# Performance work log

Measured on AMD Instinct MI355X. Metric: run time of the kernel, lower is better.

## Reference

```python
import jax, jax.numpy as jnp
import numpy as np

NB = 5          # LC kernel size (odd -> L_out == L with pad = NB//2)
S = 8           # num_sparse_LC segments
N_LEVELS = 4
K_DENSE = 3
K_LC = 3
SQ = np.float32(np.sqrt(0.5))


def haar_dec(x):
    # level-1 haar wavedec, periodization mode; x: (..., L), L even
    x0, x1 = x[..., 0::2], x[..., 1::2]
    return (x0 + x1) * SQ, (x0 - x1) * SQ  # (cA, cD)


def haar_rec(cA, cD):
    # inverse of haar_dec
    x0 = (cA + cD) * SQ
    x1 = (cA - cD) * SQ
    return jnp.stack([x0, x1], axis=-1).reshape(cA.shape[:-1] + (-1,))


def lc_apply(x, w, b):
    # cheapPartiallyUnsharedConv1d. x: (B,d,k,2,L); w: (d,k,o=2,i=2,S,NB); b: (d,k,2,S)
    L = x.shape[-1]
    p = NB // 2
    xp = jnp.pad(x, ((0, 0),) * 4 + ((p, p),))
    idx = jnp.arange(L)[:, None] + jnp.arange(NB)[None, :]      # (L, NB)
    patches = xp[..., idx]                                      # (B,d,k,2,L,NB)
    # per-segment weights: floor(L/S) repeats per segment, remainder -> last segment
    R = L // S
    seg = jnp.clip(jnp.arange(L) // R, 0, S - 1)                # (L,)
    wf = w[:, :, :, :, seg, :]                                  # (d,k,o,i,L,NB)
    bf = b[:, :, :, seg]                                        # (d,k,o,L)
    return jnp.einsum('dkoilf,bdkilf->bdkol', wf, patches) + bf


def lin_deriv(ts, ys, t):
    # derivative of linear interpolation of ys over knots ts, evaluated at t
    # ts: (T,); ys: (B,T,D); t: (T,) -> (B,T,D)
    i = jnp.clip(jnp.searchsorted(ts, t, side='right') - 1, 0, ts.shape[0] - 2)
    return (ys[:, i + 1, :] - ys[:, i, :]) / (ts[i + 1] - ts[i])[None, :, None]


def setup_inputs() -> dict:
    key = jax.random.key(0)
    ks = jax.random.split(key, 8)
    B, L, D, d, k = 16, 2048, 64, 32, 16
    dn = L >> N_LEVELS  # 128 == dense_dim
    seq = jax.random.normal(ks[0], (B, L, D), jnp.float32)
    coeffs = jax.random.normal(ks[1], (B, L, D), jnp.float32)
    time_step = jnp.arange(L, dtype=jnp.float32)
    time = jnp.arange(L, dtype=jnp.float32)
    Wg = jax.random.normal(ks[2], (D, d), jnp.float32) * (2.0 / D) ** 0.5
    Wh = jax.random.normal(ks[3], (d, D * k), jnp.float32) * (2.0 / d) ** 0.5
    dense_W = jax.random.normal(ks[4], (K_DENSE, d, k, dn, dn), jnp.float32) * (2.0 / dn) ** 0.5
    lc_w = jax.random.normal(ks[5], (N_LEVELS, K_LC, d, k, 2, 2, S, NB), jnp.float32) * (2.0 / (2 * NB)) ** 0.5
    lc_b = jax.random.uniform(ks[6], (N_LEVELS, K_LC, d, k, 2, S), jnp.float32)
    Wrev = jax.random.normal(ks[7], (d, D), jnp.float32) * (2.0 / d) ** 0.5
    return dict(seq=seq, coeffs=coeffs, time=time, time_step=time_step,
                Wg=Wg, Wh=Wh, dense_W=dense_W, lc_w=lc_w, lc_b=lc_b, Wrev=Wrev)


def reference(seq, coeffs, time, time_step, Wg, Wh, dense_W, lc_w, lc_b, Wrev):
    B, L, D = seq.shape
    d = Wg.shape[1]
    k = Wh.shape[1] // D
    der = lin_deriv(time_step, coeffs, time)                    # (B,L,D) == der_X.squeeze(-1)
    z = jax.nn.relu(seq @ Wg)                                   # (B,L,d)
    h = jax.nn.relu(z @ Wh).reshape(B, L, D, k)                 # (B,L,D,k)
    v = jnp.einsum('blDk,blD->bkl', h, der)                     # (B,k,L)

    # analysis: n_levels of level-1 haar wavedec
    ca = v
    details, approxs = [], []
    for _ in range(N_LEVELS):
        ca, cd = haar_dec(ca)
        details.append(cd)
        approxs.append(ca)

    # coarsest approx -> per-(d,k) dense stack
    cur = jnp.tile(approxs[-1][:, None, :, :], (1, d, 1, 1))    # (B,d,k,dn)
    for j in range(K_DENSE):
        cur = jnp.einsum('dktq,bdkq->bdkt', dense_W[j], cur)

    # synthesis with locally-connected refinements
    for l in reversed(range(N_LEVELS)):
        chi = jnp.tile(jnp.stack([details[l], approxs[l]], axis=2)[:, None],
                       (1, d, 1, 1, 1))                          # (B,d,k,2,Ll)
        for j in range(K_LC):
            chi = jax.nn.relu(lc_apply(chi, lc_w[l, j], lc_b[l, j]))
        # shape_correction is identity: lengths match exactly with haar/pow2
        X = chi.at[:, :, :, 1, :].add(cur)                       # add approx on channel 1
        cur = haar_rec(X[:, :, :, 1, :], X[:, :, :, 0, :])       # (B,d,k,2*Ll)

    out = jnp.sum(cur, axis=2)                                   # (B,d,L)
    U = jnp.transpose(out, (0, 2, 1)) @ Wrev                     # (B,L,D_out)
    return U
```

## Files before the change

kernel.cpp:

```cpp
#include <hip/hip_runtime.h>

#define SQC 0.70710678118654752f

typedef __attribute__((ext_vector_type(8))) short bf16x8;
typedef __attribute__((ext_vector_type(4))) float f32x4;

__device__ __forceinline__ unsigned short bf16_rne(float x) {
  unsigned int u = __float_as_uint(x);
  u += 0x7FFFu + ((u >> 16) & 1u);
  return (unsigned short)(u >> 16);
}

__global__ __launch_bounds__(256) void k_prep_all(const float* __restrict__ Wh,
                                                  unsigned short* __restrict__ WhT,
                                                  const float* __restrict__ lcw,
                                                  const float* __restrict__ lcb,
                                                  float* __restrict__ re) {
  int bid = blockIdx.x;
  if (bid < 128) {
    int i = bid * 256 + threadIdx.x;
    int n = i >> 5, dd = i & 31;
    WhT[i] = bf16_rne(Wh[dd * 1024 + n]);
    return;
  }
  int g = (bid - 128) * 256 + threadIdx.x;
  int l = g / 294912;
  int r1 = g - l * 294912;
  int dk = r1 / 576;
  int i = r1 - dk * 576;
  int j = i / 192;
  int r = i - j * 192;
  int sg = r / 24;
  int t = r - sg * 24;
  float val = 0.f;
  if (t < 20) {
    int oi = t / 5, f = t - oi * 5;
    val = lcw[((size_t)(l * 3 + j) * 512 + dk) * 160 + (oi * 8 + sg) * 5 + f];
  } else if (t < 22) {
    val = lcb[((size_t)(l * 3 + j) * 512 + dk) * 16 + (t - 20) * 8 + sg];
  }
  re[g] = val;
}

__global__ __launch_bounds__(256) void k_zv(const float* __restrict__ seq,
                                            const float* __restrict__ Wg,
                                            const float* __restrict__ coeffs,
                                            const unsigned short* __restrict__ WhT,
                                            float* __restrict__ v) {
  __shared__ unsigned short zs[64][40];
  __shared__ float ders[64][68];
  __shared__ float vout[16][68];
  const int tid = threadIdx.x;
  const int b = blockIdx.x >> 5;
  const int lblk = (blockIdx.x & 31) * 64;
  {
    const int r = tid >> 2;
    const int dq = tid & 3;
    const float4* srow = (const float4*)(seq + ((size_t)b * 2048 + lblk + r) * 64);
    float acc[8];
#pragma unroll
    for (int i = 0; i < 8; ++i) acc[i] = 0.f;
#pragma unroll 4
    for (int D4 = 0; D4 < 16; ++D4) {
      float4 s4 = srow[D4];
      const float* sp = (const float*)&s4;
#pragma unroll
      for (int q = 0; q < 4; ++q) {
        float s = sp[q];
        int D = D4 * 4 + q;
        const float* wr = Wg + D * 32 + dq * 8;
#pragma unroll
        for (int dd2 = 0; dd2 < 8; ++dd2) acc[dd2] = fmaf(s, wr[dd2], acc[dd2]);
      }
    }
    uint4 o;
    unsigned int* op = (unsigned int*)&o;
#pragma unroll
    for (int i = 0; i < 4; ++i) {
      unsigned int lo = bf16_rne(fmaxf(acc[2 * i], 0.f));
      unsigned int hi = bf16_rne(fmaxf(acc[2 * i + 1], 0.f));
      op[i] = lo | (hi << 16);
    }
    *(uint4*)&zs[r][dq * 8] = o;
  }
  for (int i = tid; i < 4096; i += 256) {
    int r = i >> 6, D = i & 63;
    int ii = min(lblk + r, 2046);
    const float* c0 = coeffs + ((size_t)b * 2048 + ii) * 64 + D;
    ders[r][D] = c0[64] - c0[0];
  }
  __syncthreads();
  const int lane = tid & 63;
  const int wv = tid >> 6;
  const int col = lane & 15, quad = lane >> 4;
  bf16x8 afrag = *(bf16x8*)&zs[wv * 16 + col][quad * 8];
  f32x4 vacc = {0.f, 0.f, 0.f, 0.f};
  const unsigned short* bptr = WhT + col * 32 + quad * 8;
  const int lrow0 = wv * 16 + quad * 4;
#pragma unroll 4
  for (int t = 0; t < 64; ++t) {
    bf16x8 bfrag = *(const bf16x8*)(bptr + t * 512);
    f32x4 c = {0.f, 0.f, 0.f, 0.f};
    c = __builtin_amdgcn_mfma_f32_16x16x32_bf16(afrag, bfrag, c, 0, 0, 0);
#pragma unroll
    for (int r = 0; r < 4; ++r)
      vacc[r] = fmaf(fmaxf(c[r], 0.f), ders[lrow0 + r][t], vacc[r]);
  }
#pragma unroll
  for (int r = 0; r < 4; ++r) vout[col][lrow0 + r] = vacc[r];
  __syncthreads();
  for (int i = tid; i < 1024; i += 256) {
    int kk = i >> 6, ll = i & 63;
    v[((size_t)b * 16 + kk) * 2048 + lblk + ll] = vout[kk][ll];
  }
}

__global__ __launch_bounds__(64) void k_haar(const float* __restrict__ v,
                                             float* __restrict__ wdet,
                                             float* __restrict__ wapp,
                                             float* __restrict__ a0T) {
  const int bk = blockIdx.x;
  const int L = threadIdx.x;
  const float* src = v + (size_t)bk * 2048 + L * 32;
  float x[32];
#pragma unroll
  for (int j = 0; j < 8; ++j) *(float4*)&x[4 * j] = ((const float4*)src)[j];
  const size_t base = (size_t)bk * 1920;
  float ca0[16], cd0[16];
#pragma unroll
  for (int i = 0; i < 16; ++i) {
    ca0[i] = (x[2 * i] + x[2 * i + 1]) * SQC;
    cd0[i] = (x[2 * i] - x[2 * i + 1]) * SQC;
  }
  {
    float* wd = wdet + base + L * 16;
    float* wa = wapp + base + L * 16;
#pragma unroll
    for (int j = 0; j < 4; ++j) {
      *(float4*)(wd + 4 * j) = *(float4*)&cd0[4 * j];
      *(float4*)(wa + 4 * j) = *(float4*)&ca0[4 * j];
    }
  }
  float ca1[8], cd1[8];
#pragma unroll
  for (int i = 0; i < 8; ++i) {
    ca1[i] = (ca0[2 * i] + ca0[2 * i + 1]) * SQC;
    cd1[i] = (ca0[2 * i] - ca0[2 * i + 1]) * SQC;
  }
  {
    float* wd = wdet + base + 1024 + L * 8;
    float* wa = wapp + base + 1024 + L * 8;
#pragma unroll
    for (int j = 0; j < 2; ++j) {
      *(float4*)(wd + 4 * j) = *(float4*)&cd1[4 * j];
      *(float4*)(wa + 4 * j) = *(float4*)&ca1[4 * j];
    }
  }
  float ca2[4], cd2[4];
#pragma unroll
  for (int i = 0; i < 4; ++i) {
    ca2[i] = (ca1[2 * i] + ca1[2 * i + 1]) * SQC;
    cd2[i] = (ca1[2 * i] - ca1[2 * i + 1]) * SQC;
  }
  *(float4*)(wdet + base + 1536 + L * 4) = *(float4*)&cd2[0];
  *(float4*)(wapp + base + 1536 + L * 4) = *(float4*)&ca2[0];
  float ca3[2], cd3[2];
#pragma unroll
  for (int i = 0; i < 2; ++i) {
    ca3[i] = (ca2[2 * i] + ca2[2 * i + 1]) * SQC;
    cd3[i] = (ca2[2 * i] - ca2[2 * i + 1]) * SQC;
  }
  *(float2*)(wdet + base + 1792 + L * 2) = *(float2*)&cd3[0];
  *(float2*)(wapp + base + 1792 + L * 2) = *(float2*)&ca3[0];
  const int k = bk & 15, bb = bk >> 4;
  a0T[((size_t)k * 128 + 2 * L) * 16 + bb] = ca3[0];
  a0T[((size_t)k * 128 + 2 * L + 1) * 16 + bb] = ca3[1];
}

__global__ __launch_bounds__(256) void k_dense3(const float* __restrict__ dW,
                                                const float* __restrict__ a0T,
                                                float* __restrict__ curd) {
  __shared__ float bufA[128 * 20];
  __shared__ float bufB[128 * 20];
  const int tid = threadIdx.x;
  const int dk = blockIdx.x;
  const int d = dk >> 4, k = dk & 15;
  {
    const float* src = a0T + (size_t)k * 2048;
    for (int i = tid; i < 2048; i += 256) {
      int q = i >> 4, b = i & 15;
      bufA[q * 20 + b] = src[i];
    }
  }
  const int t = tid & 127;
  const int bh = (tid >> 7) << 3;
  float acc[8];
  float* bin = bufA;
  float* bout = bufB;
#pragma unroll 1
  for (int j = 0; j < 3; ++j) {
    __syncthreads();
    const float* Wt = dW + ((size_t)j * 512 + dk) * 16384 + (size_t)t * 128;
#pragma unroll
    for (int i = 0; i < 8; ++i) acc[i] = 0.f;
#pragma unroll 4
    for (int q4 = 0; q4 < 32; ++q4) {
      float4 wv4 = ((const float4*)Wt)[q4];
      const float* wp = (const float*)&wv4;
#pragma unroll
      for (int qq = 0; qq < 4; ++qq) {
        int q = q4 * 4 + qq;
        float w = wp[qq];
        const float* ar = bin + q * 20 + bh;
        float4 a0 = *(const float4*)(ar);
        float4 a1 = *(const float4*)(ar + 4);
        acc[0] = fmaf(w, a0.x, acc[0]); acc[1] = fmaf(w, a0.y, acc[1]);
        acc[2] = fmaf(w, a0.z, acc[2]); acc[3] = fmaf(w, a0.w, acc[3]);
        acc[4] = fmaf(w, a1.x, acc[4]); acc[5] = fmaf(w, a1.y, acc[5]);
        acc[6] = fmaf(w, a1.z, acc[6]); acc[7] = fmaf(w, a1.w, acc[7]);
      }
    }
    if (j < 2) {
      float* orow = bout + t * 20 + bh;
      *(float4*)orow = make_float4(acc[0], acc[1], acc[2], acc[3]);
      *(float4*)(orow + 4) = make_float4(acc[4], acc[5], acc[6], acc[7]);
      float* tmp = bin; bin = bout; bout = tmp;
    }
  }
#pragma unroll
  for (int i = 0; i < 8; ++i) {
    int b = bh + i;
    curd[(((size_t)b * 32 + d) * 16 + k) * 128 + t] = acc[i];
  }
}

__device__ __forceinline__ void loadw24(float (&wl)[24], const float* p) {
#pragma unroll
  for (int i = 0; i < 6; ++i) *(float4*)&wl[4 * i] = *(const float4*)(p + 4 * i);
}

template <int P>
__device__ __forceinline__ void conv_inplace(int lane, const float (&wl)[24],
                                             float (&x0)[P], float (&x1)[P]) {
  float l00 = __shfl_up(x0[P - 2], 1), l01 = __shfl_up(x0[P - 1], 1);
  float l10 = __shfl_up(x1[P - 2], 1), l11 = __shfl_up(x1[P - 1], 1);
  float r00 = __shfl_down(x0[0], 1), r01 = __shfl_down(x0[1], 1);
  float r10 = __shfl_down(x1[0], 1), r11 = __shfl_down(x1[1], 1);
  if (lane == 0) { l00 = 0.f; l01 = 0.f; l10 = 0.f; l11 = 0.f; }
  if (lane == 63) { r00 = 0.f; r01 = 0.f; r10 = 0.f; r11 = 0.f; }
  float a0 = l00, b0 = l01, a1 = l10, b1 = l11;
#pragma unroll
  for (int i = 0; i < P; ++i) {
    float c0 = x0[i], c1 = x1[i];
    float d0 = (i + 1 < P) ? x0[i + 1] : r00;
    float d1 = (i + 1 < P) ? x1[i + 1] : r10;
    float e0 = (i + 2 < P) ? x0[i + 2] : ((i + 2 == P) ? r00 : r01);
    float e1 = (i + 2 < P) ? x1[i + 2] : ((i + 2 == P) ? r10 : r11);
    float o0 = wl[20], o1 = wl[21];
    o0 = fmaf(wl[0], a0, o0); o0 = fmaf(wl[1], b0, o0); o0 = fmaf(wl[2], c0, o0);
    o0 = fmaf(wl[3], d0, o0); o0 = fmaf(wl[4], e0, o0);
    o0 = fmaf(wl[5], a1, o0); o0 = fmaf(wl[6], b1, o0); o0 = fmaf(wl[7], c1, o0);
    o0 = fmaf(wl[8], d1, o0); o0 = fmaf(wl[9], e1, o0);
    o1 = fmaf(wl[10], a0, o1); o1 = fmaf(wl[11], b0, o1); o1 = fmaf(wl[12], c0, o1);
    o1 = fmaf(wl[13], d0, o1); o1 = fmaf(wl[14], e0, o1);
    o1 = fmaf(wl[15], a1, o1); o1 = fmaf(wl[16], b1, o1); o1 = fmaf(wl[17], c1, o1);
    o1 = fmaf(wl[18], d1, o1); o1 = fmaf(wl[19], e1, o1);
    a0 = b0; b0 = c0; a1 = b1; b1 = c1;
    x0[i] = fmaxf(o0, 0.f);
    x1[i] = fmaxf(o1, 0.f);
  }
}

template <int P>
__device__ __forceinline__ void conv3(int lane, const float* wb, int seg,
                                      float (&x0)[P], float (&x1)[P]) {
  float wl[24];
  loadw24(wl, wb + (0 * 8 + seg) * 24);
  conv_inplace<P>(lane, wl, x0, x1);
  loadw24(wl, wb + (1 * 8 + seg) * 24);
  conv_inplace<P>(lane, wl, x0, x1);
  loadw24(wl, wb + (2 * 8 + seg) * 24);
  conv_inplace<P>(lane, wl, x0, x1);
}

template <int P>
__device__ __forceinline__ void haar_rec_reg(const float (&x0)[P], const float (&x1)[P],
                                             const float (&cur)[P], float (&nxt)[2 * P]) {
#pragma unroll
  for (int i = 0; i < P; ++i) {
    float X1 = x1[i] + cur[i], X0 = x0[i];
    nxt[2 * i] = (X1 + X0) * SQC;
    nxt[2 * i + 1] = (X1 - X0) * SQC;
  }
}

template <int P>
__device__ __forceinline__ void load_chi(const float* __restrict__ wdet,
                                         const float* __restrict__ wapp,
                                         size_t off, float (&x0)[P], float (&x1)[P]) {
  if constexpr (P >= 4) {
#pragma unroll
    for (int i = 0; i < P; i += 4) {
      *(float4*)&x0[i] = *(const float4*)(wdet + off + i);
      *(float4*)&x1[i] = *(const float4*)(wapp + off + i);
    }
  } else {
#pragma unroll
    for (int i = 0; i < P; i += 2) {
      *(float2*)&x0[i] = *(const float2*)(wdet + off + i);
      *(float2*)&x1[i] = *(const float2*)(wapp + off + i);
    }
  }
}

__global__ __launch_bounds__(256, 2) void k_lc(const float* __restrict__ wdet,
                                               const float* __restrict__ wapp,
                                               const float* __restrict__ curd,
                                               const float* __restrict__ lcw_re,
                                               float* __restrict__ osum01,
                                               float* __restrict__ osum23) {
  __shared__ float wbuf[4][2][584];
  __shared__ float accb[2][2112];
  const int tid = threadIdx.x;
  const int lane = tid & 63;
  const int wv = tid >> 6;
  const int kg = blockIdx.x & 3;
  const int d = (blockIdx.x >> 2) & 31;
  const int b = blockIdx.x >> 7;
  const int k = kg * 4 + wv;
  const int bk = b * 16 + k;
  const int dk = d * 16 + k;
  const int seg = lane >> 3;
  const size_t base = (size_t)bk * 1920;

  struct StReg { float4 a, b, c; };
  auto stage_issue = [&](int l) {
    const float4* src = (const float4*)(lcw_re + ((size_t)(l * 512) + dk) * 576);
    StReg r;
    r.a = src[lane];
    r.b = src[lane + 64];
    if (lane < 16) r.c = src[lane + 128];
    return r;
  };
  auto stage_commit = [&](const StReg& r, int slot) {
    float4* dst = (float4*)wbuf[wv][slot];
    dst[lane] = r.a;
    dst[lane + 64] = r.b;
    if (lane < 16) dst[lane + 128] = r.c;
  };

  StReg r3 = stage_issue(3);
  StReg r2 = stage_issue(2);
  float c3x0[2], c3x1[2], c3[2];
  load_chi<2>(wdet, wapp, base + 1792 + lane * 2, c3x0, c3x1);
  *(float2*)&c3[0] =
      *(const float2*)(curd + (((size_t)b * 32 + d) * 16 + k) * 128 + lane * 2);
  float c2x0[4], c2x1[4];
  load_chi<4>(wdet, wapp, base + 1536 + lane * 4, c2x0, c2x1);
  stage_commit(r3, 0);

  float cur4[4];
  conv3<2>(lane, wbuf[wv][0], seg, c3x0, c3x1);
  haar_rec_reg<2>(c3x0, c3x1, c3, cur4);

  StReg r1 = stage_issue(1);
  float c1x0[8], c1x1[8];
  load_chi<8>(wdet, wapp, base + 1024 + lane * 8, c1x0, c1x1);
  stage_commit(r2, 1);

  float cur8[8];
  conv3<4>(lane, wbuf[wv][1], seg, c2x0, c2x1);
  haar_rec_reg<4>(c2x0, c2x1, cur4, cur8);

  StReg r0 = stage_issue(0);
  float c0x0[16], c0x1[16];
  load_chi<16>(wdet, wapp, base + lane * 16, c0x0, c0x1);
  stage_commit(r1, 0);

  float cur16[16];
  conv3<8>(lane, wbuf[wv][0], seg, c1x0, c1x1);
  haar_rec_reg<8>(c1x0, c1x1, cur8, cur16);
  stage_commit(r0, 1);

  {
    conv3<16>(lane, wbuf[wv][1], seg, c0x0, c0x1);
    float* arow = &accb[wv & 1][lane * 33];
    if (wv >= 2) {
#pragma unroll
      for (int i = 0; i < 16; ++i) {
        float X1 = c0x1[i] + cur16[i], X0 = c0x0[i];
        arow[2 * i] = (X1 + X0) * SQC;
        arow[2 * i + 1] = (X1 - X0) * SQC;
      }
    }
    __syncthreads();
    if (wv < 2) {
#pragma unroll
      for (int i = 0; i < 16; ++i) {
        float X1 = c0x1[i] + cur16[i], X0 = c0x0[i];
        arow[2 * i] += (X1 + X0) * SQC;
        arow[2 * i + 1] += (X1 - X0) * SQC;
      }
    }
  }
  __syncthreads();
  float* obase = (kg < 2) ? osum01 : osum23;
  float* orow = obase + ((size_t)(kg & 1) * 512 + (size_t)b * 32 + d) * 2048;
#pragma unroll
  for (int r = 0; r < 8; ++r) {
    int p = r * 256 + tid;
    int L = p >> 5, J = p & 31;
    int a = L * 33 + J;
    orow[p] = accb[0][a] + accb[1][a];
  }
}

__global__ __launch_bounds__(256) void k_final(const float* __restrict__ osum01,
                                               const float* __restrict__ osum23,
                                               const float* __restrict__ Wrev,
                                               float* __restrict__ U) {
  __shared__ float xs[64][33];
  const int tid = threadIdx.x;
  const int b = blockIdx.x >> 5;
  const int lblk = (blockIdx.x & 31) * 64;
#pragma unroll
  for (int r = 0; r < 8; ++r) {
    int p = r * 256 + tid;
    int ll = p & 63, dd = p >> 6;
    size_t off = ((size_t)b * 32 + dd) * 2048 + lblk + ll;
    xs[ll][dd] = osum01[off] + osum01[off + 1048576] +
                 osum23[off] + osum23[off + 1048576];
  }
  __syncthreads();
  const int ll = tid >> 2;
  const int Dq = tid & 3;
  float acc[16];
#pragma unroll
  for (int i = 0; i < 16; ++i) acc[i] = 0.f;
#pragma unroll 4
  for (int dd = 0; dd < 32; ++dd) {
    float x = xs[ll][dd];
    const float* wr = Wrev + dd * 64 + Dq * 16;
#pragma unroll
    for (int j = 0; j < 16; ++j) acc[j] = fmaf(x, wr[j], acc[j]);
  }
  float* o = U + ((size_t)b * 2048 + lblk + ll) * 64 + Dq * 16;
#pragma unroll
  for (int i = 0; i < 4; ++i)
    *(float4*)(o + 4 * i) =
        make_float4(acc[4 * i], acc[4 * i + 1], acc[4 * i + 2], acc[4 * i + 3]);
}

extern "C" void kernel_launch(void* const* d_in, const int* in_sizes, int n_in,
                              void* d_out, int out_size, void* d_ws, size_t ws_size,
                              hipStream_t stream) {
  const float* seq    = (const float*)d_in[0];
  const float* coeffs = (const float*)d_in[1];
  const float* Wg   = (const float*)d_in[4];
  const float* Wh   = (const float*)d_in[5];
  const float* dW   = (const float*)d_in[6];
  const float* lcw  = (const float*)d_in[7];
  const float* lcb  = (const float*)d_in[8];
  const float* Wrev = (const float*)d_in[9];
  float* out = (float*)d_out;

  float* w      = (float*)d_ws;
  float* v      = w + 1048576;
  float* a0T    = w + 1572864;
  unsigned short* WhT = (unsigned short*)(w + 1572864 + 16384);
  float* lcw_re = w + 1605632;
  float* curd   = w + 3702784;
  float* osum01 = w + 4751360;
  float* wdet   = w + 6848512;
  float* wapp   = w + 7340032;
  float* osum23 = w + 7831552;

  k_prep_all<<<4736, 256, 0, stream>>>(Wh, WhT, lcw, lcb, lcw_re);
  k_zv<<<512, 256, 0, stream>>>(seq, Wg, coeffs, WhT, v);
  k_haar<<<256, 64, 0, stream>>>(v, wdet, wapp, a0T);
  k_dense3<<<512, 256, 0, stream>>>(dW, a0T, curd);
  k_lc<<<2048, 256, 0, stream>>>(wdet, wapp, curd, lcw_re, osum01, osum23);
  k_final<<<512, 256, 0, stream>>>(osum01, osum23, Wrev, out);
}
```

Before: 260.9 us.

## Process all 16 k per block in k_lc and accumulate in registers

Each k_lc block now handles all 16 k channels for one (b,d), looping four k per wave and accumulating the reconstructed output in registers. The block then does one shared-memory reduction and a single write. This removes the four partial-sum buffers and the 4-way sum in k_final, cutting global write and read traffic. In exchange the grid shrinks from 2048 to 512 blocks, each loop iteration runs serially with less latency hiding, and launch bounds drop to one block per CU because of the added register accumulators.

```diff
diff --git a/kernel.cpp b/kernel.cpp
--- a/kernel.cpp
+++ b/kernel.cpp
@@ -313,99 +313,102 @@
   }
 }
 
-__global__ __launch_bounds__(256, 2) void k_lc(const float* __restrict__ wdet,
+__global__ __launch_bounds__(256, 1) void k_lc(const float* __restrict__ wdet,
                                                const float* __restrict__ wapp,
                                                const float* __restrict__ curd,
                                                const float* __restrict__ lcw_re,
-                                               float* __restrict__ osum01,
-                                               float* __restrict__ osum23) {
+                                               float* __restrict__ osum) {
   __shared__ float wbuf[4][2][584];
   __shared__ float accb[2][2112];
   const int tid = threadIdx.x;
   const int lane = tid & 63;
   const int wv = tid >> 6;
-  const int kg = blockIdx.x & 3;
-  const int d = (blockIdx.x >> 2) & 31;
-  const int b = blockIdx.x >> 7;
-  const int k = kg * 4 + wv;
-  const int bk = b * 16 + k;
-  const int dk = d * 16 + k;
+  const int d = blockIdx.x & 31;
+  const int b = blockIdx.x >> 5;
   const int seg = lane >> 3;
-  const size_t base = (size_t)bk * 1920;
+
+  float racc[32];
+#pragma unroll
+  for (int i = 0; i < 32; ++i) racc[i] = 0.f;
 
   struct StReg { float4 a, b, c; };
-  auto stage_issue = [&](int l) {
-    const float4* src = (const float4*)(lcw_re + ((size_t)(l * 512) + dk) * 576);
-    StReg r;
-    r.a = src[lane];
-    r.b = src[lane + 64];
-    if (lane < 16) r.c = src[lane + 128];
-    return r;
-  };
-  auto stage_commit = [&](const StReg& r, int slot) {
-    float4* dst = (float4*)wbuf[wv][slot];
-    dst[lane] = r.a;
-    dst[lane + 64] = r.b;
-    if (lane < 16) dst[lane + 128] = r.c;
-  };
-
-  StReg r3 = stage_issue(3);
-  StReg r2 = stage_issue(2);
-  float c3x0[2], c3x1[2], c3[2];
-  load_chi<2>(wdet, wapp, base + 1792 + lane * 2, c3x0, c3x1);
-  *(float2*)&c3[0] =
-      *(const float2*)(curd + (((size_t)b * 32 + d) * 16 + k) * 128 + lane * 2);
-  float c2x0[4], c2x1[4];
-  load_chi<4>(wdet, wapp, base + 1536 + lane * 4, c2x0, c2x1);
-  stage_commit(r3, 0);
-
-  float cur4[4];
-  conv3<2>(lane, wbuf[wv][0], seg, c3x0, c3x1);
-  haar_rec_reg<2>(c3x0, c3x1, c3, cur4);
-
-  StReg r1 = stage_issue(1);
-  float c1x0[8], c1x1[8];
-  load_chi<8>(wdet, wapp, base + 1024 + lane * 8, c1x0, c1x1);
-  stage_commit(r2, 1);
-
-  float cur8[8];
-  conv3<4>(lane, wbuf[wv][1], seg, c2x0, c2x1);
-  haar_rec_reg<4>(c2x0, c2x1, cur4, cur8);
-
-  StReg r0 = stage_issue(0);
-  float c0x0[16], c0x1[16];
-  load_chi<16>(wdet, wapp, base + lane * 16, c0x0, c0x1);
-  stage_commit(r1, 0);
-
-  float cur16[16];
-  conv3<8>(lane, wbuf[wv][0], seg, c1x0, c1x1);
-  haar_rec_reg<8>(c1x0, c1x1, cur8, cur16);
-  stage_commit(r0, 1);
-
-  {
+
+#pragma unroll 1
+  for (int c = 0; c < 4; ++c) {
+    const int k = wv * 4 + c;
+    const int bk = b * 16 + k;
+    const int dk = d * 16 + k;
+    const size_t base = (size_t)bk * 1920;
+
+    auto stage_issue = [&](int l) {
+      const float4* src = (const float4*)(lcw_re + ((size_t)(l * 512) + dk) * 576);
+      StReg r;
+      r.a = src[lane];
+      r.b = src[lane + 64];
+      if (lane < 16) r.c = src[lane + 128];
+      return r;
+    };
+    auto stage_commit = [&](const StReg& r, int slot) {
+      float4* dst = (float4*)wbuf[wv][slot];
+      dst[lane] = r.a;
+      dst[lane + 64] = r.b;
+      if (lane < 16) dst[lane + 128] = r.c;
+    };
+
+    StReg r3 = stage_issue(3);
+    StReg r2 = stage_issue(2);
+    float c3x0[2], c3x1[2], c3[2];
+    load_chi<2>(wdet, wapp, base + 1792 + lane * 2, c3x0, c3x1);
+    *(float2*)&c3[0] =
+        *(const float2*)(curd + (((size_t)b * 32 + d) * 16 + k) * 128 + lane * 2);
+    float c2x0[4], c2x1[4];
+    load_chi<4>(wdet, wapp, base + 1536 + lane * 4, c2x0, c2x1);
+    stage_commit(r3, 0);
+
+    float cur4[4];
+    conv3<2>(lane, wbuf[wv][0], seg, c3x0, c3x1);
+    haar_rec_reg<2>(c3x0, c3x1, c3, cur4);
+
+    StReg r1 = stage_issue(1);
+    float c1x0[8], c1x1[8];
+    load_chi<8>(wdet, wapp, base + 1024 + lane * 8, c1x0, c1x1);
+    stage_commit(r2, 1);
+
+    float cur8[8];
+    conv3<4>(lane, wbuf[wv][1], seg, c2x0, c2x1);
+    haar_rec_reg<4>(c2x0, c2x1, cur4, cur8);
+
+    StReg r0 = stage_issue(0);
+    float c0x0[16], c0x1[16];
+    load_chi<16>(wdet, wapp, base + lane * 16, c0x0, c0x1);
+    stage_commit(r1, 0);
+
+    float cur16[16];
+    conv3<8>(lane, wbuf[wv][0], seg, c1x0, c1x1);
+    haar_rec_reg<8>(c1x0, c1x1, cur8, cur16);
+    stage_commit(r0, 1);
+
     conv3<16>(lane, wbuf[wv][1], seg, c0x0, c0x1);
-    float* arow = &accb[wv & 1][lane * 33];
-    if (wv >= 2) {
-#pragma unroll
-      for (int i = 0; i < 16; ++i) {
-        float X1 = c0x1[i] + cur16[i], X0 = c0x0[i];
-        arow[2 * i] = (X1 + X0) * SQC;
-        arow[2 * i + 1] = (X1 - X0) * SQC;
-      }
-    }
-    __syncthreads();
-    if (wv < 2) {
-#pragma unroll
-      for (int i = 0; i < 16; ++i) {
-        float X1 = c0x1[i] + cur16[i], X0 = c0x0[i];
-        arow[2 * i] += (X1 + X0) * SQC;
-        arow[2 * i + 1] += (X1 - X0) * SQC;
-      }
-    }
+#pragma unroll
+    for (int i = 0; i < 16; ++i) {
+      float X1 = c0x1[i] + cur16[i], X0 = c0x0[i];
+      racc[2 * i] += (X1 + X0) * SQC;
+      racc[2 * i + 1] += (X1 - X0) * SQC;
+    }
+  }
+
+  float* arow = &accb[wv & 1][lane * 33];
+  if (wv >= 2) {
+#pragma unroll
+    for (int i = 0; i < 32; ++i) arow[i] = racc[i];
   }
   __syncthreads();
-  float* obase = (kg < 2) ? osum01 : osum23;
-  float* orow = obase + ((size_t)(kg & 1) * 512 + (size_t)b * 32 + d) * 2048;
+  if (wv < 2) {
+#pragma unroll
+    for (int i = 0; i < 32; ++i) arow[i] += racc[i];
+  }
+  __syncthreads();
+  float* orow = osum + ((size_t)b * 32 + d) * 2048;
 #pragma unroll
   for (int r = 0; r < 8; ++r) {
     int p = r * 256 + tid;
@@ -415,8 +418,7 @@
   }
 }
 
-__global__ __launch_bounds__(256) void k_final(const float* __restrict__ osum01,
-                                               const float* __restrict__ osum23,
+__global__ __launch_bounds__(256) void k_final(const float* __restrict__ osum,
                                                const float* __restrict__ Wrev,
                                                float* __restrict__ U) {
   __shared__ float xs[64][33];
@@ -427,9 +429,7 @@
   for (int r = 0; r < 8; ++r) {
     int p = r * 256 + tid;
     int ll = p & 63, dd = p >> 6;
-    size_t off = ((size_t)b * 32 + dd) * 2048 + lblk + ll;
-    xs[ll][dd] = osum01[off] + osum01[off + 1048576] +
-                 osum23[off] + osum23[off + 1048576];
+    xs[ll][dd] = osum[((size_t)b * 32 + dd) * 2048 + lblk + ll];
   }
   __syncthreads();
   const int ll = tid >> 2;
@@ -470,15 +470,14 @@
   unsigned short* WhT = (unsigned short*)(w + 1572864 + 16384);
   float* lcw_re = w + 1605632;
   float* curd   = w + 3702784;
-  float* osum01 = w + 4751360;
+  float* osum   = w + 4751360;
   float* wdet   = w + 6848512;
   float* wapp   = w + 7340032;
-  float* osum23 = w + 7831552;
 
   k_prep_all<<<4736, 256, 0, stream>>>(Wh, WhT, lcw, lcb, lcw_re);
   k_zv<<<512, 256, 0, stream>>>(seq, Wg, coeffs, WhT, v);
   k_haar<<<256, 64, 0, stream>>>(v, wdet, wapp, a0T);
   k_dense3<<<512, 256, 0, stream>>>(dW, a0T, curd);
-  k_lc<<<2048, 256, 0, stream>>>(wdet, wapp, curd, lcw_re, osum01, osum23);
-  k_final<<<512, 256, 0, stream>>>(osum01, osum23, Wrev, out);
-}
+  k_lc<<<512, 256, 0, stream>>>(wdet, wapp, curd, lcw_re, osum);
+  k_final<<<512, 256, 0, stream>>>(osum, Wrev, out);
+}
```

Result: no change. 258.5 us (-0.9%).
